# Performance work log

Hardware: AMD Instinct MI355X
Metric: run time of the kernel (lower is better)

## Reference

```python
import jax, jax.numpy as jnp
import numpy as np

B = 64
T0_V = 512   # existing timesteps already in the graph memory
TAU_V = 128  # new timesteps inserted this call
NTOT = T0_V + TAU_V  # 640 == graph_size
FEAT = 256
K = 16       # causal temporal window (edges j->i for j in [i-K, i))


def _build_edges():
    # per-batch causal edges, then offset by b*NTOT into the flat graph
    src_l, dst_l = [], []
    for off in range(1, K + 1):
        ii = np.arange(off, NTOT)
        src_l.append(ii - off)
        dst_l.append(ii)
    src = np.concatenate(src_l)
    dst = np.concatenate(dst_l)
    boff = (np.arange(B) * NTOT)[:, None]
    edge_src = (src[None, :] + boff).reshape(-1)
    edge_dst = (dst[None, :] + boff).reshape(-1)
    return jnp.asarray(edge_src, jnp.int32), jnp.asarray(edge_dst, jnp.int32)


def setup_inputs() -> dict:
    key = jax.random.key(0)
    ks = jax.random.split(key, 8)
    x = jax.random.normal(ks[0], (B, TAU_V, FEAT), jnp.float32)
    nodes = 0.1 * jax.random.normal(ks[1], (B, NTOT, FEAT), jnp.float32)
    edge_src, edge_dst = _build_edges()
    E = edge_src.shape[0]
    edge_weight = jnp.ones((E,), jnp.float32)
    sc = 1.0 / np.sqrt(FEAT)
    W1_self = sc * jax.random.normal(ks[2], (FEAT, FEAT), jnp.float32)
    W1_nbr = sc * jax.random.normal(ks[3], (FEAT, FEAT), jnp.float32)
    b1 = jnp.zeros((FEAT,), jnp.float32)
    W2_self = sc * jax.random.normal(ks[4], (FEAT, FEAT), jnp.float32)
    W2_nbr = sc * jax.random.normal(ks[5], (FEAT, FEAT), jnp.float32)
    b2 = jnp.zeros((FEAT,), jnp.float32)
    return {"x": x, "nodes": nodes, "edge_weight": edge_weight,
            "W1_self": W1_self, "W1_nbr": W1_nbr, "b1": b1,
            "W2_self": W2_self, "W2_nbr": W2_nbr, "b2": b2,
            "edge_src": edge_src, "edge_dst": edge_dst,
            "T0": T0_V, "tau": TAU_V}


def reference(x, nodes, edge_weight, W1_self, W1_nbr, b1, W2_self, W2_nbr, b2,
              edge_src, edge_dst, T0, tau):
    Bv, t, feat = x.shape
    ntot = T0 + tau
    # scatter new observations into the node memory (uniform taus -> dense slice)
    nodes = nodes.at[:, T0:T0 + tau, :].set(x)
    # adj normalization: values / values.detach() == 1 in the forward pass
    w = edge_weight / jax.lax.stop_gradient(edge_weight)
    # flatten per-batch ragged graphs (regular here since taus are uniform)
    flat = nodes[:, :ntot].reshape(Bv * ntot, feat)  # [B*ntot, feat]
    nseg = Bv * ntot

    def gconv(h, Ws, Wn, b):
        msg = h[edge_src] * w[:, None]                       # [E, d] gather
        agg = jax.ops.segment_sum(msg, edge_dst, num_segments=nseg)
        return jnp.tanh(h @ Ws + agg @ Wn + b)

    h = gconv(flat, W1_self, W1_nbr, b1)
    h = gconv(h, W2_self, W2_nbr, b2)
    # gather outputs for the newly-inserted nodes -> [B, tau, out_feat]
    out_idx = (jnp.arange(Bv)[:, None] * ntot + T0 + jnp.arange(tau)[None, :]).reshape(-1)
    mx_dense = h[out_idx].reshape(Bv, tau, -1)
    return mx_dense
```

## Files before the change

### kernel.cpp

```cpp
#include <hip/hip_runtime.h>
#include <hip/hip_bf16.h>


namespace {

constexpr int BQ    = 64;
constexpr int FEATC = 256;
constexpr int M1 = 144;
constexpr int M2 = 128;

using ushort = unsigned short;
using short8 = __attribute__((ext_vector_type(8))) short;
using f32x4  = __attribute__((ext_vector_type(4))) float;

__device__ __forceinline__ ushort f2bf(float f) {
  union { float f; unsigned u; } v{f};
  unsigned r = v.u + 0x7FFFu + ((v.u >> 16) & 1u);
  return (ushort)(r >> 16);
}
__device__ __forceinline__ float bf2f(ushort h) {
  union { unsigned u; float f; } v{(unsigned)h << 16};
  return v.f;
}
__device__ __forceinline__ void split2(float v, ushort& hi, ushort& lo) {
  hi = f2bf(v);
  lo = f2bf(v - bf2f(hi));
}
__device__ __forceinline__ float tanh_fast(float x) {
  const float e = __builtin_amdgcn_exp2f(x * 2.8853900817779268f);
  return 1.0f - 2.0f * __builtin_amdgcn_rcpf(1.0f + e);
}
__device__ __forceinline__ void gl_lds16(const ushort* g, ushort* l) {
  __builtin_amdgcn_global_load_lds(
      (const __attribute__((address_space(1))) void*)g,
      (__attribute__((address_space(3))) void*)l, 16, 0, 0);
}

__device__ __forceinline__ size_t frag_idx(int row, int k, int s) {
  return ((size_t)(((row >> 4) * 16 + (k >> 5)) * 2 + s)) * 512
       + ((k >> 3) & 3) * 128 + (row & 15) * 8 + (k & 7);
}
__device__ __forceinline__ int lofs(int row_l, int k, int s) {
  return ((k >> 5) * 2 + s) * 512 + ((k >> 3) & 3) * 128 + row_l * 8 + (k & 7);
}

__global__ __launch_bounds__(256) void prep_fused(
    const float* __restrict__ x, const float* __restrict__ nodes,
    const float* __restrict__ W1s, const float* __restrict__ W1n,
    const float* __restrict__ W2s, const float* __restrict__ W2n,
    ushort* __restrict__ A1F, ushort* __restrict__ WF1,
    ushort* __restrict__ WF2) {
  __shared__ ushort lds_o[16384];
  __shared__ float tile[64][65];
  const int blk = blockIdx.x;
  if (blk < 576) {
    const int G = 4 * (blk % 144) + (blk / 144);
    const int b = G / 9, c = G % 9, f = threadIdx.x;
    const int t0 = c * 16, i0 = 496 + t0;
    const float* nb = nodes + ((size_t)b * 640) * FEATC + f;
    const float* xb = x     + ((size_t)b * 128) * FEATC + f;

    float v[32];
    #pragma unroll
    for (int d = 0; d < 32; ++d) {
      const int i = i0 - 16 + d;
      v[d] = (i < 512) ? nb[(size_t)i * FEATC] : xb[(size_t)(i - 512) * FEATC];
    }
    float win = 0.f;
    #pragma unroll
    for (int d = 0; d < 16; ++d) win += v[d];

    #pragma unroll
    for (int tt = 0; tt < 16; ++tt) {
      ushort hi, lo;
      split2(v[16 + tt], hi, lo);
      lds_o[lofs(tt, f, 0)] = hi;
      lds_o[lofs(tt, f, 1)] = lo;
      split2(win, hi, lo);
      lds_o[lofs(tt, 256 + f, 0)] = hi;
      lds_o[lofs(tt, 256 + f, 1)] = lo;
      win += v[16 + tt] - v[tt];
    }
    __syncthreads();
    ushort* dst = A1F + (size_t)G * 16384;
    #pragma unroll
    for (int it = 0; it < 8; ++it) {
      const int idx = it * 256 + threadIdx.x;
      *(short8*)(dst + idx * 8) = *(const short8*)(lds_o + idx * 8);
    }
  } else {
    const int w = blk - 576;
    const int z = w >> 4, rem = w & 15;
    const int k0 = (rem >> 2) * 64, n0 = (rem & 3) * 64;
    const float* src = (z == 0) ? W1s : (z == 1) ? W1n : (z == 2) ? W2s : W2n;
    ushort* dst = (z < 2) ? WF1 : WF2;
    const int koff = (z & 1) * 256;
    const int c = threadIdx.x & 63, r4 = threadIdx.x >> 6;
    #pragma unroll
    for (int p = 0; p < 16; ++p) {
      const int k = r4 + p * 4;
      tile[k][c] = src[(size_t)(k0 + k) * FEATC + n0 + c];
    }
    __syncthreads();
    #pragma unroll
    for (int p = 0; p < 16; ++p) {
      const int n = r4 + p * 4;
      ushort hi, lo;
      split2(tile[c][n], hi, lo);
      dst[frag_idx(n0 + n, koff + k0 + c, 0)] = hi;
      dst[frag_idx(n0 + n, koff + k0 + c, 1)] = lo;
    }
  }
}

#define GLOAD(dst, ptr)                                                      \
  asm volatile("global_load_dwordx4 %0, %1, off"                             \
               : "=v"(dst) : "v"(ptr) : "memory")

#define WAITV(n) do {                                                        \
  asm volatile("s_waitcnt vmcnt(" #n ")" ::: "memory");                      \
  __builtin_amdgcn_sched_barrier(0);                                         \
} while (0)

#define MF(a, b, c) c = __builtin_amdgcn_mfma_f32_16x16x32_bf16(a, b, c, 0, 0, 0)

#define STAGEA(jn, kb) do {                                                  \
  gl_lds16(srcu0 + (kb) * 1024, sbase + (jn) * 5120 + u0 * 512);             \
  gl_lds16(srcu1 + (kb) * 1024, sbase + (jn) * 5120 + u1 * 512);             \
  if (g3) gl_lds16(srcu2 + (kb) * 1024, sbase + (jn) * 5120 + u2 * 512);     \
} while (0)

#define WAITW do { if (g3) { WAITV(5); } else { WAITV(4); } } while (0)

#define COMPJ2(j, WH, WL) do {                                               \
  const ushort* bp_ = sbase + (j) * 5120 + lane * 8;                         \
  const short8 a0h = *(const short8*)(bp_ + 0 * 512);                        \
  const short8 a0l = *(const short8*)(bp_ + 1 * 512);                        \
  const short8 a1h = *(const short8*)(bp_ + 2 * 512);                        \
  const short8 a1l = *(const short8*)(bp_ + 3 * 512);                        \
  const short8 a2h = *(const short8*)(bp_ + 4 * 512);                        \
  const short8 a2l = *(const short8*)(bp_ + 5 * 512);                        \
  const short8 a3h = *(const short8*)(bp_ + 6 * 512);                        \
  const short8 a3l = *(const short8*)(bp_ + 7 * 512);                        \
  const short8 a4h = *(const short8*)(bp_ + 8 * 512);                        \
  const short8 a4l = *(const short8*)(bp_ + 9 * 512);                        \
  __builtin_amdgcn_s_setprio(1);                                            \
  MF(a0h, WH, acc[0]); MF(a1h, WH, acc[1]); MF(a2h, WH, acc[2]);             \
  MF(a3h, WH, acc[3]); MF(a4h, WH, acc[4]);                                  \
  MF(a0h, WL, acc[0]); MF(a1h, WL, acc[1]); MF(a2h, WL, acc[2]);             \
  MF(a3h, WL, acc[3]); MF(a4h, WL, acc[4]);                                  \
  MF(a0l, WH, acc[0]); MF(a1l, WH, acc[1]); MF(a2l, WH, acc[2]);             \
  MF(a3l, WH, acc[3]); MF(a4l, WH, acc[4]);                                  \
  __builtin_amdgcn_s_setprio(0);                                            \
  __builtin_amdgcn_sched_barrier(0);                                        \
} while (0)

__global__ __launch_bounds__(256, 2) void gemm1_fused(
    const ushort* __restrict__ A, const ushort* __restrict__ W,
    const float* __restrict__ bias, ushort* __restrict__ A2F) {
  __shared__ __align__(16) unsigned char ldsmem[54528];
  ushort* sbase = (ushort*)ldsmem;
  float (*hvt)[68] = (float(*)[68])ldsmem;
  ushort* outb = (ushort*)(ldsmem + 21760);

  const int tid = threadIdx.x;
  const int wave = tid >> 6, lane = tid & 63;
  const int lr = lane & 15, kg = lane >> 4;
  const int mx2 = blockIdx.x, ny = blockIdx.y;
  const int b = mx2 >> 1, half = mx2 & 1;
  const int rgA0 = 9 * b + 4 * half;
  const int n0 = ny * 64;
  const int ngw = ny * 4 + wave;

  const bool g3 = (wave < 2);
  const int uw = g3 ? wave * 3 : 6 + (wave - 2) * 2;
  const int u0 = uw, u1 = uw + 1, u2 = g3 ? uw + 2 : uw + 1;
  auto srcA = [&](int u) {
    return A + ((size_t)(rgA0 + (u >> 1)) * 32 + (u & 1)) * 512 + lane * 8;
  };
  const ushort* srcu0 = srcA(u0);
  const ushort* srcu1 = srcA(u1);
  const ushort* srcu2 = srcA(u2);

  const ushort* bW = W + (size_t)ngw * 16384 + lane * 8;

  f32x4 acc[5] = {};
  short8 w0h, w0l, w1h, w1l, w2h, w2l;

  STAGEA(0, 0); GLOAD(w0h, bW);        GLOAD(w0l, bW + 512);
  STAGEA(1, 1); GLOAD(w1h, bW + 1024); GLOAD(w1l, bW + 1536);

#define STEP(k, j, jn, WH, WL, NWH, NWL)                                     \
  WAITW; __builtin_amdgcn_s_barrier();                                       \
  COMPJ2(j, WH, WL);                                                         \
  STAGEA(jn, (k) + 2);                                                       \
  GLOAD(NWH, bW + ((k) + 2) * 1024); GLOAD(NWL, bW + ((k) + 2) * 1024 + 512)

  STEP(0, 0, 2, w0h, w0l, w2h, w2l);
  STEP(1, 1, 0, w1h, w1l, w0h, w0l);
  STEP(2, 2, 1, w2h, w2l, w1h, w1l);
  STEP(3, 0, 2, w0h, w0l, w2h, w2l);
  STEP(4, 1, 0, w1h, w1l, w0h, w0l);
  STEP(5, 2, 1, w2h, w2l, w1h, w1l);
  STEP(6, 0, 2, w0h, w0l, w2h, w2l);
  STEP(7, 1, 0, w1h, w1l, w0h, w0l);
  STEP(8, 2, 1, w2h, w2l, w1h, w1l);
  STEP(9, 0, 2, w0h, w0l, w2h, w2l);
  STEP(10, 1, 0, w1h, w1l, w0h, w0l);
  STEP(11, 2, 1, w2h, w2l, w1h, w1l);
  STEP(12, 0, 2, w0h, w0l, w2h, w2l);
  STEP(13, 1, 0, w1h, w1l, w0h, w0l);
  WAITW; __builtin_amdgcn_s_barrier();
  COMPJ2(2, w2h, w2l);
  WAITV(0); __builtin_amdgcn_s_barrier();
  COMPJ2(0, w0h, w0l);
#undef STEP

  __syncthreads();

  const float bv = bias[n0 + wave * 16 + lr];
  #pragma unroll
  for (int fr = 0; fr < 5; ++fr)
    #pragma unroll
    for (int r = 0; r < 4; ++r)
      hvt[fr * 16 + kg * 4 + r][wave * 16 + lr] = tanh_fast(acc[fr][r] + bv);
  __syncthreads();

  {
    const int col = tid & 63, q = tid >> 6;
    float hv[32];
    #pragma unroll
    for (int d = 0; d < 32; ++d) hv[d] = hvt[q * 16 + d][col];
    float win = 0.f;
    #pragma unroll
    for (int d = 0; d < 16; ++d) win += hv[d];

    const int su = ((q * 4 + (col >> 5)) * 2) * 512
                 + ((col >> 3) & 3) * 128 + (col & 7);
    const int wu = ((q * 4 + 2 + (col >> 5)) * 2) * 512
                 + ((col >> 3) & 3) * 128 + (col & 7);
    #pragma unroll
    for (int tt = 0; tt < 16; ++tt) {
      ushort hi, lo;
      split2(hv[16 + tt], hi, lo);
      outb[su + tt * 8]       = hi;
      outb[su + tt * 8 + 512] = lo;
      split2(win, hi, lo);
      outb[wu + tt * 8]       = hi;
      outb[wu + tt * 8 + 512] = lo;
      win += hv[16 + tt] - hv[tt];
    }
  }
  __syncthreads();

  const int rg20 = 4 * mx2;
  #pragma unroll
  for (int it = 0; it < 8; ++it) {
    const int lin = it * 2048 + tid * 8;
    const int u = lin >> 9, w = lin & 511;
    const int uq = u >> 3, ukbl = (u >> 1) & 3, us = u & 1;
    const int KB = (ukbl < 2) ? (2 * ny + ukbl) : (8 + 2 * ny + (ukbl - 2));
    const size_t dst = ((size_t)((rg20 + uq) * 16 + KB) * 2 + us) * 512 + w;
    *(short8*)(A2F + dst) = *(const short8*)(outb + lin);
  }
}

struct FB { short8 ah0, ah1, al0, al1, b10, b11, b20, b21; };

#define LOADI(Q, tt) do {                                                    \
  GLOAD(Q.ah0, baseA00 + (tt) * 1024);                                       \
  GLOAD(Q.ah1, baseA10 + (tt) * 1024);                                       \
  GLOAD(Q.al0, baseA01 + (tt) * 1024);                                       \
  GLOAD(Q.al1, baseA11 + (tt) * 1024);                                       \
  GLOAD(Q.b10, baseW0h + (tt) * 1024);                                       \
  GLOAD(Q.b11, baseW1h + (tt) * 1024);                                       \
  GLOAD(Q.b20, baseW0l + (tt) * 1024);                                       \
  GLOAD(Q.b21, baseW1l + (tt) * 1024);                                       \
} while (0)

#define COMP(Q) do {                                                         \
  __builtin_amdgcn_s_setprio(1);                                             \
  MF(Q.ah0, Q.b10, acc00); MF(Q.ah0, Q.b11, acc01);                          \
  MF(Q.ah1, Q.b10, acc10); MF(Q.ah1, Q.b11, acc11);                          \
  MF(Q.ah0, Q.b20, acc00); MF(Q.ah0, Q.b21, acc01);                          \
  MF(Q.ah1, Q.b20, acc10); MF(Q.ah1, Q.b21, acc11);                          \
  MF(Q.al0, Q.b10, acc00); MF(Q.al0, Q.b11, acc01);                          \
  MF(Q.al1, Q.b10, acc10); MF(Q.al1, Q.b11, acc11);                          \
  __builtin_amdgcn_s_setprio(0);                                             \
  __builtin_amdgcn_sched_barrier(0);                                         \
} while (0)

__global__ __launch_bounds__(256, 2) void gemm_mfma(
    const ushort* __restrict__ A, const ushort* __restrict__ W,
    const float* __restrict__ bias, float* __restrict__ out) {
  const int t = threadIdx.x;
  const int wave = t >> 6, lane = t & 63;
  const int lr = lane & 15, kg = lane >> 4;
  const int m0 = blockIdx.x * 64 + (wave >> 1) * 32;
  const int n0 = blockIdx.y * 64 + (wave & 1) * 32;
  const int rg0 = m0 >> 4, ng0 = n0 >> 4;

  const ushort* baseA00 = A + ((size_t)((rg0 + 0) * 32 + 0)) * 512 + lane * 8;
  const ushort* baseA01 = A + ((size_t)((rg0 + 0) * 32 + 1)) * 512 + lane * 8;
  const ushort* baseA10 = A + ((size_t)((rg0 + 1) * 32 + 0)) * 512 + lane * 8;
  const ushort* baseA11 = A + ((size_t)((rg0 + 1) * 32 + 1)) * 512 + lane * 8;
  const ushort* baseW0h = W + ((size_t)((ng0 + 0) * 32 + 0)) * 512 + lane * 8;
  const ushort* baseW0l = W + ((size_t)((ng0 + 0) * 32 + 1)) * 512 + lane * 8;
  const ushort* baseW1h = W + ((size_t)((ng0 + 1) * 32 + 0)) * 512 + lane * 8;
  const ushort* baseW1l = W + ((size_t)((ng0 + 1) * 32 + 1)) * 512 + lane * 8;

  f32x4 acc00 = {}, acc01 = {}, acc10 = {}, acc11 = {};
  FB q0, q1, q2, q3, q4;

  LOADI(q0, 0); LOADI(q1, 1); LOADI(q2, 2); LOADI(q3, 3); LOADI(q4, 4);
  WAITV(32); COMP(q0); LOADI(q0, 5);
  WAITV(32); COMP(q1); LOADI(q1, 6);
  WAITV(32); COMP(q2); LOADI(q2, 7);
  WAITV(32); COMP(q3); LOADI(q3, 8);
  WAITV(32); COMP(q4); LOADI(q4, 9);
  WAITV(32); COMP(q0); LOADI(q0, 10);
  WAITV(32); COMP(q1); LOADI(q1, 11);
  WAITV(32); COMP(q2); LOADI(q2, 12);
  WAITV(32); COMP(q3); LOADI(q3, 13);
  WAITV(32); COMP(q4); LOADI(q4, 14);
  WAITV(32); COMP(q0); LOADI(q0, 15);
  WAITV(32); COMP(q1);
  WAITV(24); COMP(q2);
  WAITV(16); COMP(q3);
  WAITV(8);  COMP(q4);
  WAITV(0);  COMP(q0);

  const float bv0 = bias[n0 + lr];
  const float bv1 = bias[n0 + 16 + lr];
  auto epi = [&](const f32x4& a, int mt, int nt, float bv) {
    #pragma unroll
    for (int r = 0; r < 4; ++r) {
      const int row = m0 + mt * 16 + kg * 4 + r;
      const int col = n0 + nt * 16 + lr;
      out[(size_t)row * FEATC + col] = tanh_fast(a[r] + bv);
    }
  };
  epi(acc00, 0, 0, bv0);
  epi(acc01, 0, 1, bv1);
  epi(acc10, 1, 0, bv0);
  epi(acc11, 1, 1, bv1);
}

}

extern "C" void kernel_launch(void* const* d_in, const int* in_sizes, int n_in,
                              void* d_out, int out_size, void* d_ws, size_t ws_size,
                              hipStream_t stream) {
  const float* x     = (const float*)d_in[0];
  const float* nodes = (const float*)d_in[1];
  const float* W1s = (const float*)d_in[3];
  const float* W1n = (const float*)d_in[4];
  const float* b1  = (const float*)d_in[5];
  const float* W2s = (const float*)d_in[6];
  const float* W2n = (const float*)d_in[7];
  const float* b2  = (const float*)d_in[8];
  float* out = (float*)d_out;

  const size_t a1_sz = (size_t)BQ * M1 * 1024;
  const size_t a2_sz = (size_t)BQ * M2 * 1024;
  const size_t wf_sz = (size_t)16 * 16 * 2 * 512;
  const size_t need = (a1_sz + a2_sz + 2 * wf_sz) * sizeof(ushort);
  if (ws_size < need) return;

  ushort* p = (ushort*)d_ws;
  ushort* A1F = p; p += a1_sz;
  ushort* A2F = p; p += a2_sz;
  ushort* WF1 = p; p += wf_sz;
  ushort* WF2 = p; p += wf_sz;

  prep_fused<<<640, 256, 0, stream>>>(x, nodes, W1s, W1n, W2s, W2n,
                                      A1F, WF1, WF2);
  gemm1_fused<<<dim3(BQ * 2, FEATC / 64), 256, 0, stream>>>(A1F, WF1, b1, A2F);
  gemm_mfma<<<dim3((BQ * M2) / 64, FEATC / 64), 256, 0, stream>>>(
      A2F, WF2, b2, out);
}
```

Baseline: 37.37 us.

## Stage shared A tiles in LDS for second GEMM with triple buffering

```diff
diff --git a/kernel.cpp b/kernel.cpp
--- a/kernel.cpp
+++ b/kernel.cpp
@@ -265,85 +265,93 @@
   }
 }
 
-struct FB { short8 ah0, ah1, al0, al1, b10, b11, b20, b21; };
-
-#define LOADI(Q, tt) do {                                                    \
-  GLOAD(Q.ah0, baseA00 + (tt) * 1024);                                       \
-  GLOAD(Q.ah1, baseA10 + (tt) * 1024);                                       \
-  GLOAD(Q.al0, baseA01 + (tt) * 1024);                                       \
-  GLOAD(Q.al1, baseA11 + (tt) * 1024);                                       \
-  GLOAD(Q.b10, baseW0h + (tt) * 1024);                                       \
-  GLOAD(Q.b11, baseW1h + (tt) * 1024);                                       \
-  GLOAD(Q.b20, baseW0l + (tt) * 1024);                                       \
-  GLOAD(Q.b21, baseW1l + (tt) * 1024);                                       \
-} while (0)
-
-#define COMP(Q) do {                                                         \
-  __builtin_amdgcn_s_setprio(1);                                             \
-  MF(Q.ah0, Q.b10, acc00); MF(Q.ah0, Q.b11, acc01);                          \
-  MF(Q.ah1, Q.b10, acc10); MF(Q.ah1, Q.b11, acc11);                          \
-  MF(Q.ah0, Q.b20, acc00); MF(Q.ah0, Q.b21, acc01);                          \
-  MF(Q.ah1, Q.b20, acc10); MF(Q.ah1, Q.b21, acc11);                          \
-  MF(Q.al0, Q.b10, acc00); MF(Q.al0, Q.b11, acc01);                          \
-  MF(Q.al1, Q.b10, acc10); MF(Q.al1, Q.b11, acc11);                          \
-  __builtin_amdgcn_s_setprio(0);                                             \
-  __builtin_amdgcn_sched_barrier(0);                                         \
-} while (0)
-
-__global__ __launch_bounds__(256, 2) void gemm_mfma(
+#define STAGE2(jn, kb) do {                                                  \
+  gl_lds16(srcv0 + (kb) * 1024, sb2 + (jn) * 4096 + v0 * 512);               \
+  gl_lds16(srcv1 + (kb) * 1024, sb2 + (jn) * 4096 + v1 * 512);               \
+} while (0)
+
+#define COMPK(j, WH, WL) do {                                                \
+  const ushort* bp_ = sb2 + (j) * 4096 + lane * 8;                           \
+  const short8 a0h = *(const short8*)(bp_ + 0 * 512);                        \
+  const short8 a0l = *(const short8*)(bp_ + 1 * 512);                        \
+  const short8 a1h = *(const short8*)(bp_ + 2 * 512);                        \
+  const short8 a1l = *(const short8*)(bp_ + 3 * 512);                        \
+  const short8 a2h = *(const short8*)(bp_ + 4 * 512);                        \
+  const short8 a2l = *(const short8*)(bp_ + 5 * 512);                        \
+  const short8 a3h = *(const short8*)(bp_ + 6 * 512);                        \
+  const short8 a3l = *(const short8*)(bp_ + 7 * 512);                        \
+  __builtin_amdgcn_s_setprio(1);                                            \
+  MF(a0h, WH, acc[0]); MF(a1h, WH, acc[1]);                                  \
+  MF(a2h, WH, acc[2]); MF(a3h, WH, acc[3]);                                  \
+  MF(a0h, WL, acc[0]); MF(a1h, WL, acc[1]);                                  \
+  MF(a2h, WL, acc[2]); MF(a3h, WL, acc[3]);                                  \
+  MF(a0l, WH, acc[0]); MF(a1l, WH, acc[1]);                                  \
+  MF(a2l, WH, acc[2]); MF(a3l, WH, acc[3]);                                  \
+  __builtin_amdgcn_s_setprio(0);                                            \
+  __builtin_amdgcn_sched_barrier(0);                                        \
+} while (0)
+
+__global__ __launch_bounds__(256, 2) void gemm2_lds(
     const ushort* __restrict__ A, const ushort* __restrict__ W,
     const float* __restrict__ bias, float* __restrict__ out) {
-  const int t = threadIdx.x;
-  const int wave = t >> 6, lane = t & 63;
+  __shared__ __align__(16) ushort sb2[3 * 4096];
+
+  const int tid = threadIdx.x;
+  const int wave = tid >> 6, lane = tid & 63;
   const int lr = lane & 15, kg = lane >> 4;
-  const int m0 = blockIdx.x * 64 + (wave >> 1) * 32;
-  const int n0 = blockIdx.y * 64 + (wave & 1) * 32;
-  const int rg0 = m0 >> 4, ng0 = n0 >> 4;
-
-  const ushort* baseA00 = A + ((size_t)((rg0 + 0) * 32 + 0)) * 512 + lane * 8;
-  const ushort* baseA01 = A + ((size_t)((rg0 + 0) * 32 + 1)) * 512 + lane * 8;
-  const ushort* baseA10 = A + ((size_t)((rg0 + 1) * 32 + 0)) * 512 + lane * 8;
-  const ushort* baseA11 = A + ((size_t)((rg0 + 1) * 32 + 1)) * 512 + lane * 8;
-  const ushort* baseW0h = W + ((size_t)((ng0 + 0) * 32 + 0)) * 512 + lane * 8;
-  const ushort* baseW0l = W + ((size_t)((ng0 + 0) * 32 + 1)) * 512 + lane * 8;
-  const ushort* baseW1h = W + ((size_t)((ng0 + 1) * 32 + 0)) * 512 + lane * 8;
-  const ushort* baseW1l = W + ((size_t)((ng0 + 1) * 32 + 1)) * 512 + lane * 8;
-
-  f32x4 acc00 = {}, acc01 = {}, acc10 = {}, acc11 = {};
-  FB q0, q1, q2, q3, q4;
-
-  LOADI(q0, 0); LOADI(q1, 1); LOADI(q2, 2); LOADI(q3, 3); LOADI(q4, 4);
-  WAITV(32); COMP(q0); LOADI(q0, 5);
-  WAITV(32); COMP(q1); LOADI(q1, 6);
-  WAITV(32); COMP(q2); LOADI(q2, 7);
-  WAITV(32); COMP(q3); LOADI(q3, 8);
-  WAITV(32); COMP(q4); LOADI(q4, 9);
-  WAITV(32); COMP(q0); LOADI(q0, 10);
-  WAITV(32); COMP(q1); LOADI(q1, 11);
-  WAITV(32); COMP(q2); LOADI(q2, 12);
-  WAITV(32); COMP(q3); LOADI(q3, 13);
-  WAITV(32); COMP(q4); LOADI(q4, 14);
-  WAITV(32); COMP(q0); LOADI(q0, 15);
-  WAITV(32); COMP(q1);
-  WAITV(24); COMP(q2);
-  WAITV(16); COMP(q3);
-  WAITV(8);  COMP(q4);
-  WAITV(0);  COMP(q0);
-
-  const float bv0 = bias[n0 + lr];
-  const float bv1 = bias[n0 + 16 + lr];
-  auto epi = [&](const f32x4& a, int mt, int nt, float bv) {
+  const int mx = blockIdx.x, ny = blockIdx.y;
+  const int rg0 = mx * 4;
+  const int ngw = ny * 4 + wave;
+  const int n0col = ngw * 16;
+
+  const int v0 = wave * 2, v1 = wave * 2 + 1;
+  auto srcA = [&](int u) {
+    return A + ((size_t)(rg0 + (u >> 1)) * 32 + (u & 1)) * 512 + lane * 8;
+  };
+  const ushort* srcv0 = srcA(v0);
+  const ushort* srcv1 = srcA(v1);
+  const ushort* bW = W + (size_t)ngw * 16384 + lane * 8;
+
+  f32x4 acc[4] = {};
+  short8 w0h, w0l, w1h, w1l, w2h, w2l;
+
+  STAGE2(0, 0); GLOAD(w0h, bW);        GLOAD(w0l, bW + 512);
+  STAGE2(1, 1); GLOAD(w1h, bW + 1024); GLOAD(w1l, bW + 1536);
+
+#define STEP2(k, j, jn, WH, WL, NWH, NWL)                                    \
+  WAITV(4); __builtin_amdgcn_s_barrier();                                    \
+  COMPK(j, WH, WL);                                                          \
+  STAGE2(jn, (k) + 2);                                                       \
+  GLOAD(NWH, bW + ((k) + 2) * 1024); GLOAD(NWL, bW + ((k) + 2) * 1024 + 512)
+
+  STEP2(0, 0, 2, w0h, w0l, w2h, w2l);
+  STEP2(1, 1, 0, w1h, w1l, w0h, w0l);
+  STEP2(2, 2, 1, w2h, w2l, w1h, w1l);
+  STEP2(3, 0, 2, w0h, w0l, w2h, w2l);
+  STEP2(4, 1, 0, w1h, w1l, w0h, w0l);
+  STEP2(5, 2, 1, w2h, w2l, w1h, w1l);
+  STEP2(6, 0, 2, w0h, w0l, w2h, w2l);
+  STEP2(7, 1, 0, w1h, w1l, w0h, w0l);
+  STEP2(8, 2, 1, w2h, w2l, w1h, w1l);
+  STEP2(9, 0, 2, w0h, w0l, w2h, w2l);
+  STEP2(10, 1, 0, w1h, w1l, w0h, w0l);
+  STEP2(11, 2, 1, w2h, w2l, w1h, w1l);
+  STEP2(12, 0, 2, w0h, w0l, w2h, w2l);
+  STEP2(13, 1, 0, w1h, w1l, w0h, w0l);
+  WAITV(4); __builtin_amdgcn_s_barrier();
+  COMPK(2, w2h, w2l);
+  WAITV(0); __builtin_amdgcn_s_barrier();
+  COMPK(0, w0h, w0l);
+#undef STEP2
+
+  const float bv = bias[n0col + lr];
+  #pragma unroll
+  for (int fr = 0; fr < 4; ++fr)
     #pragma unroll
     for (int r = 0; r < 4; ++r) {
-      const int row = m0 + mt * 16 + kg * 4 + r;
-      const int col = n0 + nt * 16 + lr;
-      out[(size_t)row * FEATC + col] = tanh_fast(a[r] + bv);
-    }
-  };
-  epi(acc00, 0, 0, bv0);
-  epi(acc01, 0, 1, bv1);
-  epi(acc10, 1, 0, bv0);
-  epi(acc11, 1, 1, bv1);
+      const int row = mx * 64 + fr * 16 + kg * 4 + r;
+      out[(size_t)row * FEATC + n0col + lr] = tanh_fast(acc[fr][r] + bv);
+    }
 }
 
 }
@@ -376,6 +384,6 @@
   prep_fused<<<640, 256, 0, stream>>>(x, nodes, W1s, W1n, W2s, W2n,
                                       A1F, WF1, WF2);
   gemm1_fused<<<dim3(BQ * 2, FEATC / 64), 256, 0, stream>>>(A1F, WF1, b1, A2F);
-  gemm_mfma<<<dim3((BQ * M2) / 64, FEATC / 64), 256, 0, stream>>>(
+  gemm2_lds<<<dim3((BQ * M2) / 64, FEATC / 64), 256, 0, stream>>>(
       A2F, WF2, b2, out);
 }
```

New measurement: 35.77 us (median of 2 runs). 1.04x faster.
